# Optimization experiments

Measured on AMD Instinct MI355X. Metric: run time of the kernel, lower is better.

## Reference

```python
import jax, jax.numpy as jnp
import numpy as np

TMSG = 15  # max_len - 1


def setup_inputs() -> dict:
    key = jax.random.key(0)
    ks = jax.random.split(key, 8)
    B, T_in, E, H, V = 4096, 4, 256, 512, 32000
    s = lambda k, shape: jax.random.normal(k, shape, jnp.float32) * 0.05
    return {
        "inp": jax.random.normal(ks[0], (B, T_in, E), jnp.float32),
        "Wx0": s(ks[1], (E, 4 * H)),
        "Wh0": s(ks[2], (H, 4 * H)),
        "b0": jnp.zeros((4 * H,), jnp.float32),
        "Wx1": s(ks[3], (H, 4 * H)),
        "Wh1": s(ks[4], (H, 4 * H)),
        "b1": jnp.zeros((4 * H,), jnp.float32),
        "Wd": s(ks[5], (H, V)),
        "bd": jnp.zeros((V,), jnp.float32),
    }


def _lstm_step(x, h, c, Wx, Wh, b):
    # Keras LSTMCell gate order: i, f, g(cell), o
    z = x @ Wx + h @ Wh + b
    i, f, g, o = jnp.split(z, 4, axis=-1)
    c = jax.nn.sigmoid(f) * c + jax.nn.sigmoid(i) * jnp.tanh(g)
    h = jax.nn.sigmoid(o) * jnp.tanh(c)
    return h, c


def reference(inp, Wx0, Wh0, b0, Wx1, Wh1, b1, Wd, bd):
    B = inp.shape[0]
    H = Wh0.shape[0]
    z = jnp.zeros((B, H), inp.dtype)

    def scan_fn(carry, x_t):
        h0, c0, h1, c1 = carry
        h0, c0 = _lstm_step(x_t, h0, c0, Wx0, Wh0, b0)
        h1, c1 = _lstm_step(h0, h1, c1, Wx1, Wh1, b1)
        return (h0, c0, h1, c1), None

    # NOTE: source bug resets initial_state to None every step, so each of the
    # max_len-1 steps runs the identical stacked LSTM from zero state; we run it once.
    (h0, c0, h1, c1), _ = jax.lax.scan(scan_fn, (z, z, z, z), jnp.swapaxes(inp, 0, 1))
    out = h1  # (B, H) last-step output of top cell

    log_probs = jax.nn.log_softmax(out @ Wd + bd, axis=-1)  # (B, V)
    probs = jnp.exp(log_probs)
    entropy = -jnp.sum(probs * log_probs, axis=-1)  # (B,)

    keys = jax.random.split(jax.random.key(42), TMSG)
    samples = jax.vmap(lambda k: jax.random.categorical(k, log_probs, axis=-1))(keys)  # (T, B)
    lp = log_probs[jnp.arange(B)[None, :], samples]  # (T, B) log_prob of sampled chars
    ent = jnp.broadcast_to(entropy[None], (TMSG, B))  # (T, B)

    message = samples.T  # (B, T)
    message = jnp.concatenate([message, jnp.zeros_like(message)], axis=1)  # (B, 2T)
    state_h = jnp.stack([h0, c0])  # keras unpack quirk: states[0] = [h, c] of cell 0
    return (message, lp, ent, state_h)
```

## Files before the change

### kernel.cpp

```cpp
#include <hip/hip_runtime.h>
#include <stdint.h>
#include <math.h>

#define BB 4096
#define HH 512
#define VV 32000
#define NT 15
#define STF 2097152

struct KeysArg { uint32_t w[2*NT]; };

__host__ __device__ inline void tf2x32(uint32_t k0, uint32_t k1,
                                       uint32_t x0, uint32_t x1,
                                       uint32_t& o0, uint32_t& o1) {
  uint32_t ks2 = k0 ^ k1 ^ 0x1BD11BDAu;
  x0 += k0; x1 += k1;
#define TF_R(r) { x0 += x1; x1 = (x1 << (r)) | (x1 >> (32 - (r))); x1 ^= x0; }
  TF_R(13) TF_R(15) TF_R(26) TF_R(6)
  x0 += k1; x1 += ks2 + 1u;
  TF_R(17) TF_R(29) TF_R(16) TF_R(24)
  x0 += ks2; x1 += k0 + 2u;
  TF_R(13) TF_R(15) TF_R(26) TF_R(6)
  x0 += k0; x1 += k1 + 3u;
  TF_R(17) TF_R(29) TF_R(16) TF_R(24)
  x0 += k1; x1 += ks2 + 4u;
  TF_R(13) TF_R(15) TF_R(26) TF_R(6)
  x0 += ks2; x1 += k0 + 5u;
#undef TF_R
  o0 = x0; o1 = x1;
}

__device__ inline float gumbel32(uint32_t bits) {
  float f = __uint_as_float((bits >> 9) | 0x3f800000u) - 1.0f;
  f = fmaxf(f, 1.17549435e-38f);
  return -logf(-logf(f));
}

__global__ __launch_bounds__(256)
void gemm2_kernel(const float* __restrict__ A1, int lda1, int K1,
                  const float* __restrict__ A2, int lda2, int K2,
                  const float* __restrict__ W1, const float* __restrict__ W2,
                  int ldw,
                  const float* __restrict__ bias,
                  float* __restrict__ C, int ldc)
{
  __shared__ float As[16][128];
  __shared__ float Ws[16][128];
  const int tid = threadIdx.x;
  const int m0 = blockIdx.y * 128;
  const int n0 = blockIdx.x * 128;
  const int tx = tid & 15, ty = tid >> 4;
  float acc[8][8];
  #pragma unroll
  for (int i = 0; i < 8; ++i)
    #pragma unroll
    for (int j = 0; j < 8; ++j) acc[i][j] = 0.0f;

  const int kt1 = K1 >> 4;
  const int kt2 = A2 ? (K2 >> 4) : 0;
  const int sr = tid >> 1, sc = (tid & 1) * 8;
  const int wk = tid >> 4, wn = (tid & 15) * 8;

  for (int kt = 0; kt < kt1 + kt2; ++kt) {
    const float* A; int lda; const float* W; int k0;
    if (kt < kt1) { A = A1; lda = lda1; W = W1; k0 = kt << 4; }
    else          { A = A2; lda = lda2; W = W2; k0 = (kt - kt1) << 4; }
    const float* asrc = A + (size_t)(m0 + sr) * lda + (k0 + sc);
    float4 av0 = *(const float4*)asrc;
    float4 av1 = *(const float4*)(asrc + 4);
    const float* wsrc = W + (size_t)(k0 + wk) * ldw + (n0 + wn);
    float4 wv0 = *(const float4*)wsrc;
    float4 wv1 = *(const float4*)(wsrc + 4);
    As[sc+0][sr]=av0.x; As[sc+1][sr]=av0.y; As[sc+2][sr]=av0.z; As[sc+3][sr]=av0.w;
    As[sc+4][sr]=av1.x; As[sc+5][sr]=av1.y; As[sc+6][sr]=av1.z; As[sc+7][sr]=av1.w;
    *(float4*)&Ws[wk][wn]   = wv0;
    *(float4*)&Ws[wk][wn+4] = wv1;
    __syncthreads();
    #pragma unroll
    for (int kk = 0; kk < 16; ++kk) {
      float4 a0 = *(const float4*)&As[kk][ty*8];
      float4 a1 = *(const float4*)&As[kk][ty*8+4];
      float4 b0 = *(const float4*)&Ws[kk][tx*8];
      float4 b1 = *(const float4*)&Ws[kk][tx*8+4];
      float ar[8] = {a0.x,a0.y,a0.z,a0.w,a1.x,a1.y,a1.z,a1.w};
      float br[8] = {b0.x,b0.y,b0.z,b0.w,b1.x,b1.y,b1.z,b1.w};
      #pragma unroll
      for (int i = 0; i < 8; ++i)
        #pragma unroll
        for (int j = 0; j < 8; ++j)
          acc[i][j] = fmaf(ar[i], br[j], acc[i][j]);
    }
    __syncthreads();
  }
  #pragma unroll
  for (int i = 0; i < 8; ++i) {
    const int m = m0 + ty*8 + i;
    float* dst = C + (size_t)m * ldc + (n0 + tx*8);
    float4 o0, o1;
    o0.x = acc[i][0] + bias[n0+tx*8+0];
    o0.y = acc[i][1] + bias[n0+tx*8+1];
    o0.z = acc[i][2] + bias[n0+tx*8+2];
    o0.w = acc[i][3] + bias[n0+tx*8+3];
    o1.x = acc[i][4] + bias[n0+tx*8+4];
    o1.y = acc[i][5] + bias[n0+tx*8+5];
    o1.z = acc[i][6] + bias[n0+tx*8+6];
    o1.w = acc[i][7] + bias[n0+tx*8+7];
    *(float4*)dst       = o0;
    *(float4*)(dst + 4) = o1;
  }
}

__global__ __launch_bounds__(256)
void gate_kernel(const float* __restrict__ z, const float* __restrict__ cin,
                 float* __restrict__ hout, float* __restrict__ cout,
                 float* __restrict__ sh, float* __restrict__ sc)
{
  int idx = blockIdx.x * 256 + threadIdx.x;
  int b = idx >> 9, j = idx & 511;
  const float* zr = z + (size_t)b * 2048;
  float zi = zr[j], zf = zr[j+512], zg = zr[j+1024], zo = zr[j+1536];
  float si = 1.0f/(1.0f+expf(-zi));
  float sf = 1.0f/(1.0f+expf(-zf));
  float so = 1.0f/(1.0f+expf(-zo));
  float c = sf * cin[idx] + si * tanhf(zg);
  float h = so * tanhf(c);
  cout[idx] = c; hout[idx] = h;
  if (sh) { sh[idx] = h; sc[idx] = c; }
}

__global__ __launch_bounds__(256)
void rowstat_kernel(const float* __restrict__ logits,
                    float* __restrict__ rowM, float* __restrict__ rowLS,
                    float* __restrict__ rowEnt)
{
  const int row = blockIdx.x;
  const float* x = logits + (size_t)row * VV;
  const int tid = threadIdx.x;
  float m = -INFINITY;
  for (int v = tid; v < VV; v += 256) m = fmaxf(m, x[v]);
  #pragma unroll
  for (int off = 32; off; off >>= 1) m = fmaxf(m, __shfl_down(m, off));
  __shared__ float sm[4], ssum[4], swsum[4];
  if ((tid & 63) == 0) sm[tid >> 6] = m;
  __syncthreads();
  m = fmaxf(fmaxf(sm[0], sm[1]), fmaxf(sm[2], sm[3]));
  float s = 0.0f, w = 0.0f;
  for (int v = tid; v < VV; v += 256) {
    float d = x[v] - m;
    float e = expf(d);
    s += e; w += d * e;
  }
  #pragma unroll
  for (int off = 32; off; off >>= 1) { s += __shfl_down(s, off); w += __shfl_down(w, off); }
  if ((tid & 63) == 0) { ssum[tid >> 6] = s; swsum[tid >> 6] = w; }
  __syncthreads();
  if (tid == 0) {
    s = ssum[0]+ssum[1]+ssum[2]+ssum[3];
    w = swsum[0]+swsum[1]+swsum[2]+swsum[3];
    float ls = logf(s);
    rowM[row] = m; rowLS[row] = ls; rowEnt[row] = ls - w / s;
  }
}

__global__ __launch_bounds__(256)
void sample_kernel(const float* __restrict__ logits,
                   const float* __restrict__ rowM, const float* __restrict__ rowLS,
                   const float* __restrict__ rowEnt,
                   float* __restrict__ out,
                   KeysArg keys, int bbase)
{
  const int l = blockIdx.x;
  const int b = bbase + l;
  const float* x = logits + (size_t)l * VV;
  const float m = rowM[l], ls = rowLS[l];

  float bv[NT];
  uint32_t bi[NT];
  #pragma unroll
  for (int t = 0; t < NT; ++t) { bv[t] = -INFINITY; bi[t] = 0; }

  const uint32_t pbase = (uint32_t)b * (uint32_t)VV;
  for (int v = threadIdx.x; v < VV; v += 256) {
    const float lp = (x[v] - m) - ls;
    const uint32_t p = pbase + (uint32_t)v;
    #pragma unroll
    for (int t = 0; t < NT; ++t) {
      uint32_t o0, o1;
      tf2x32(keys.w[2*t], keys.w[2*t+1], 0u, p, o0, o1);
      float g = gumbel32(o0 ^ o1) + lp;
      if (g > bv[t]) { bv[t] = g; bi[t] = (uint32_t)v; }
    }
  }

  __shared__ float rv[NT][4];
  __shared__ uint32_t ri[NT][4];
  const int lane = threadIdx.x & 63, wq = threadIdx.x >> 6;
  #pragma unroll
  for (int t = 0; t < NT; ++t) {
    float v = bv[t]; uint32_t idx = bi[t];
    #pragma unroll
    for (int off = 32; off; off >>= 1) {
      float ov = __shfl_down(v, off);
      uint32_t oi = __shfl_down(idx, off);
      if (ov > v || (ov == v && oi < idx)) { v = ov; idx = oi; }
    }
    if (lane == 0) { rv[t][wq] = v; ri[t][wq] = idx; }
  }
  __syncthreads();
  if (threadIdx.x < NT) {
    const int t = threadIdx.x;
    float v = rv[t][0]; uint32_t idx = ri[t][0];
    #pragma unroll
    for (int q = 1; q < 4; ++q) {
      float ov = rv[t][q]; uint32_t oi = ri[t][q];
      if (ov > v || (ov == v && oi < idx)) { v = ov; idx = oi; }
    }
    out[(size_t)b * 30 + t]      = (float)idx;
    out[(size_t)b * 30 + 15 + t] = 0.0f;
    out[122880 + (size_t)t * BB + b] = (x[idx] - m) - ls;
    out[184320 + (size_t)t * BB + b] = rowEnt[l];
  }
}

extern "C" void kernel_launch(void* const* d_in, const int* in_sizes, int n_in,
                              void* d_out, int out_size, void* d_ws, size_t ws_size,
                              hipStream_t stream)
{
  const float* inp = (const float*)d_in[0];
  const float* Wx0 = (const float*)d_in[1];
  const float* Wh0 = (const float*)d_in[2];
  const float* b0v = (const float*)d_in[3];
  const float* Wx1 = (const float*)d_in[4];
  const float* Wh1 = (const float*)d_in[5];
  const float* b1v = (const float*)d_in[6];
  const float* Wd  = (const float*)d_in[7];
  const float* bdv = (const float*)d_in[8];
  float* out = (float*)d_out;
  float* ws = (float*)d_ws;

  float* h0 = ws;
  float* c0 = ws + (size_t)STF;
  float* h1 = ws + (size_t)2*STF;
  float* c1 = ws + (size_t)3*STF;
  float* z  = ws + (size_t)4*STF;
  float* rowM  = ws + (size_t)8*STF;
  float* rowLS = rowM + 4096;
  float* rowEnt = rowLS + 4096;
  float* logits = ws + (size_t)8*STF + 16384;

  size_t ws_floats = ws_size / 4;
  size_t base = (size_t)8*STF + 16384;
  int CH = 4096;
  while (CH > 128 && base + (size_t)CH*VV > ws_floats) CH >>= 1;

  hipMemsetAsync(ws, 0, (size_t)4*STF*sizeof(float), stream);

  for (int t = 0; t < 4; ++t) {
    gemm2_kernel<<<dim3(2048/128, 4096/128), 256, 0, stream>>>(
        inp + t*256, 1024, 256, h0, 512, 512, Wx0, Wh0, 2048, b0v, z, 2048);
    gate_kernel<<<STF/256, 256, 0, stream>>>(z, c0, h0, c0,
        (t==3) ? out + 245760 : (float*)nullptr,
        (t==3) ? out + 245760 + STF : (float*)nullptr);
    gemm2_kernel<<<dim3(2048/128, 4096/128), 256, 0, stream>>>(
        h0, 512, 512, h1, 512, 512, Wx1, Wh1, 2048, b1v, z, 2048);
    gate_kernel<<<STF/256, 256, 0, stream>>>(z, c1, h1, c1, (float*)nullptr, (float*)nullptr);
  }

  KeysArg ka;
  for (int t = 0; t < NT; ++t) {
    uint32_t o0, o1;
    tf2x32(0u, 42u, 0u, (uint32_t)t, o0, o1);
    ka.w[2*t] = o0; ka.w[2*t+1] = o1;
  }

  const int nch = 4096 / CH;
  for (int c = 0; c < nch; ++c) {
    int bbase = c * CH;
    gemm2_kernel<<<dim3(VV/128, CH/128), 256, 0, stream>>>(
        h1 + (size_t)bbase*512, 512, 512, nullptr, 0, 0, Wd, nullptr, VV, bdv,
        logits, VV);
    rowstat_kernel<<<CH, 256, 0, stream>>>(logits, rowM, rowLS, rowEnt);
    sample_kernel<<<CH, 256, 0, stream>>>(logits, rowM, rowLS, rowEnt, out, ka, bbase);
  }
}
```

Measured before the change: 8.231 ms.

## Double-buffer GEMM with K=32 tiles and split sampling per token with threshold pruning

The GEMM moves to 32-wide K tiles and prefetches the next tile into registers while computing the current one. The sampling kernel now launches one block per (row, token) pair instead of looping over all 15 tokens in one block. It also skips the double-log Gumbel evaluation and the logit read whenever the raw uniform falls below a threshold derived from the current best, on the basis that such candidates cannot win. This cuts the transcendental cost of sampling but re-reads each logits row 15 times, and the threshold bound (log-prob <= 0 with a 0.999999 safety factor) could alter exact sampling ties in edge cases.

```diff
diff --git a/kernel.cpp b/kernel.cpp
--- a/kernel.cpp
+++ b/kernel.cpp
@@ -30,12 +30,6 @@
   o0 = x0; o1 = x1;
 }
 
-__device__ inline float gumbel32(uint32_t bits) {
-  float f = __uint_as_float((bits >> 9) | 0x3f800000u) - 1.0f;
-  f = fmaxf(f, 1.17549435e-38f);
-  return -logf(-logf(f));
-}
-
 __global__ __launch_bounds__(256)
 void gemm2_kernel(const float* __restrict__ A1, int lda1, int K1,
                   const float* __restrict__ A2, int lda2, int K2,
@@ -44,8 +38,8 @@
                   const float* __restrict__ bias,
                   float* __restrict__ C, int ldc)
 {
-  __shared__ float As[16][128];
-  __shared__ float Ws[16][128];
+  __shared__ float As[32][128];
+  __shared__ float Ws[32][128];
   const int tid = threadIdx.x;
   const int m0 = blockIdx.y * 128;
   const int n0 = blockIdx.x * 128;
@@ -56,42 +50,68 @@
     #pragma unroll
     for (int j = 0; j < 8; ++j) acc[i][j] = 0.0f;
 
-  const int kt1 = K1 >> 4;
-  const int kt2 = A2 ? (K2 >> 4) : 0;
-  const int sr = tid >> 1, sc = (tid & 1) * 8;
+  const int kt1 = K1 >> 5;
+  const int ktT = kt1 + (A2 ? (K2 >> 5) : 0);
+  const int ar = tid >> 1, ac = (tid & 1) * 16;
   const int wk = tid >> 4, wn = (tid & 15) * 8;
 
-  for (int kt = 0; kt < kt1 + kt2; ++kt) {
+  float4 a0q, a1q, a2q, a3q, w0q, w1q, w2q, w3q;
+
+  auto LOAD = [&](int kt) {
     const float* A; int lda; const float* W; int k0;
-    if (kt < kt1) { A = A1; lda = lda1; W = W1; k0 = kt << 4; }
-    else          { A = A2; lda = lda2; W = W2; k0 = (kt - kt1) << 4; }
-    const float* asrc = A + (size_t)(m0 + sr) * lda + (k0 + sc);
-    float4 av0 = *(const float4*)asrc;
-    float4 av1 = *(const float4*)(asrc + 4);
+    if (kt < kt1) { A = A1; lda = lda1; W = W1; k0 = kt << 5; }
+    else          { A = A2; lda = lda2; W = W2; k0 = (kt - kt1) << 5; }
+    const float* asrc = A + (size_t)(m0 + ar) * lda + (k0 + ac);
+    a0q = *(const float4*)asrc;
+    a1q = *(const float4*)(asrc + 4);
+    a2q = *(const float4*)(asrc + 8);
+    a3q = *(const float4*)(asrc + 12);
     const float* wsrc = W + (size_t)(k0 + wk) * ldw + (n0 + wn);
-    float4 wv0 = *(const float4*)wsrc;
-    float4 wv1 = *(const float4*)(wsrc + 4);
-    As[sc+0][sr]=av0.x; As[sc+1][sr]=av0.y; As[sc+2][sr]=av0.z; As[sc+3][sr]=av0.w;
-    As[sc+4][sr]=av1.x; As[sc+5][sr]=av1.y; As[sc+6][sr]=av1.z; As[sc+7][sr]=av1.w;
-    *(float4*)&Ws[wk][wn]   = wv0;
-    *(float4*)&Ws[wk][wn+4] = wv1;
-    __syncthreads();
-    #pragma unroll
-    for (int kk = 0; kk < 16; ++kk) {
+    w0q = *(const float4*)wsrc;
+    w1q = *(const float4*)(wsrc + 4);
+    const float* wsrc2 = W + (size_t)(k0 + wk + 16) * ldw + (n0 + wn);
+    w2q = *(const float4*)wsrc2;
+    w3q = *(const float4*)(wsrc2 + 4);
+  };
+  auto STORE = [&]() {
+    float av[16] = {a0q.x,a0q.y,a0q.z,a0q.w, a1q.x,a1q.y,a1q.z,a1q.w,
+                    a2q.x,a2q.y,a2q.z,a2q.w, a3q.x,a3q.y,a3q.z,a3q.w};
+    #pragma unroll
+    for (int j = 0; j < 16; ++j) As[ac + j][ar] = av[j];
+    *(float4*)&Ws[wk][wn]        = w0q;
+    *(float4*)&Ws[wk][wn + 4]    = w1q;
+    *(float4*)&Ws[wk + 16][wn]   = w2q;
+    *(float4*)&Ws[wk + 16][wn+4] = w3q;
+  };
+
+  LOAD(0);
+  STORE();
+  __syncthreads();
+
+  for (int kt = 0; kt < ktT; ++kt) {
+    const bool more = (kt + 1 < ktT);
+    if (more) LOAD(kt + 1);
+    #pragma unroll
+    for (int kk = 0; kk < 32; ++kk) {
       float4 a0 = *(const float4*)&As[kk][ty*8];
       float4 a1 = *(const float4*)&As[kk][ty*8+4];
       float4 b0 = *(const float4*)&Ws[kk][tx*8];
       float4 b1 = *(const float4*)&Ws[kk][tx*8+4];
-      float ar[8] = {a0.x,a0.y,a0.z,a0.w,a1.x,a1.y,a1.z,a1.w};
-      float br[8] = {b0.x,b0.y,b0.z,b0.w,b1.x,b1.y,b1.z,b1.w};
+      float ar8[8] = {a0.x,a0.y,a0.z,a0.w,a1.x,a1.y,a1.z,a1.w};
+      float br8[8] = {b0.x,b0.y,b0.z,b0.w,b1.x,b1.y,b1.z,b1.w};
       #pragma unroll
       for (int i = 0; i < 8; ++i)
         #pragma unroll
         for (int j = 0; j < 8; ++j)
-          acc[i][j] = fmaf(ar[i], br[j], acc[i][j]);
-    }
-    __syncthreads();
-  }
+          acc[i][j] = fmaf(ar8[i], br8[j], acc[i][j]);
+    }
+    if (more) {
+      __syncthreads();
+      STORE();
+      __syncthreads();
+    }
+  }
+
   #pragma unroll
   for (int i = 0; i < 8; ++i) {
     const int m = m0 + ty*8 + i;
@@ -169,50 +189,56 @@
                    float* __restrict__ out,
                    KeysArg keys, int bbase)
 {
-  const int l = blockIdx.x;
+  const int l = blockIdx.x / NT;
+  const int t = blockIdx.x % NT;
   const int b = bbase + l;
   const float* x = logits + (size_t)l * VV;
   const float m = rowM[l], ls = rowLS[l];
-
-  float bv[NT];
-  uint32_t bi[NT];
-  #pragma unroll
-  for (int t = 0; t < NT; ++t) { bv[t] = -INFINITY; bi[t] = 0; }
+  const uint32_t k0 = keys.w[2*t], k1 = keys.w[2*t+1];
+
+  float bv = -INFINITY;
+  uint32_t bi = 0;
+  float thr = 1.0f;
 
   const uint32_t pbase = (uint32_t)b * (uint32_t)VV;
   for (int v = threadIdx.x; v < VV; v += 256) {
-    const float lp = (x[v] - m) - ls;
-    const uint32_t p = pbase + (uint32_t)v;
-    #pragma unroll
-    for (int t = 0; t < NT; ++t) {
-      uint32_t o0, o1;
-      tf2x32(keys.w[2*t], keys.w[2*t+1], 0u, p, o0, o1);
-      float g = gumbel32(o0 ^ o1) + lp;
-      if (g > bv[t]) { bv[t] = g; bi[t] = (uint32_t)v; }
-    }
-  }
-
-  __shared__ float rv[NT][4];
-  __shared__ uint32_t ri[NT][4];
+    uint32_t o0, o1;
+    tf2x32(k0, k1, 0u, pbase + (uint32_t)v, o0, o1);
+    const uint32_t bits = o0 ^ o1;
+    const float uf = __uint_as_float((bits >> 9) | 0x3f800000u);
+    if (uf >= thr) {
+      float u = fmaxf(uf - 1.0f, 1.17549435e-38f);
+      float g = -logf(-logf(u));
+      float lp = (x[v] - m) - ls;
+      float cand = g + lp;
+      if (cand > bv) {
+        bv = cand; bi = (uint32_t)v;
+        float T = bv + ls;
+        float us = expf(-expf(-T));
+        thr = 1.0f + us * 0.999999f;
+      }
+    }
+  }
+
+  __shared__ float rv[4];
+  __shared__ uint32_t ri[4];
   const int lane = threadIdx.x & 63, wq = threadIdx.x >> 6;
-  #pragma unroll
-  for (int t = 0; t < NT; ++t) {
-    float v = bv[t]; uint32_t idx = bi[t];
+  {
+    float v = bv; uint32_t idx = bi;
     #pragma unroll
     for (int off = 32; off; off >>= 1) {
       float ov = __shfl_down(v, off);
       uint32_t oi = __shfl_down(idx, off);
       if (ov > v || (ov == v && oi < idx)) { v = ov; idx = oi; }
     }
-    if (lane == 0) { rv[t][wq] = v; ri[t][wq] = idx; }
+    if (lane == 0) { rv[wq] = v; ri[wq] = idx; }
   }
   __syncthreads();
-  if (threadIdx.x < NT) {
-    const int t = threadIdx.x;
-    float v = rv[t][0]; uint32_t idx = ri[t][0];
+  if (threadIdx.x == 0) {
+    float v = rv[0]; uint32_t idx = ri[0];
     #pragma unroll
     for (int q = 1; q < 4; ++q) {
-      float ov = rv[t][q]; uint32_t oi = ri[t][q];
+      float ov = rv[q]; uint32_t oi = ri[q];
       if (ov > v || (ov == v && oi < idx)) { v = ov; idx = oi; }
     }
     out[(size_t)b * 30 + t]      = (float)idx;
@@ -280,6 +306,6 @@
         h1 + (size_t)bbase*512, 512, 512, nullptr, 0, 0, Wd, nullptr, VV, bdv,
         logits, VV);
     rowstat_kernel<<<CH, 256, 0, stream>>>(logits, rowM, rowLS, rowEnt);
-    sample_kernel<<<CH, 256, 0, stream>>>(logits, rowM, rowLS, rowEnt, out, ka, bbase);
-  }
-}
+    sample_kernel<<<CH * NT, 256, 0, stream>>>(logits, rowM, rowLS, rowEnt, out, ka, bbase);
+  }
+}
```

New measurement: 24.33 ms. 2.96x slower.
